# Performance work log

Measured on AMD Instinct MI355X. Metric: run time of the kernel, lower is better.

The kernel has to match this reference:

```python
import jax, jax.numpy as jnp
import numpy as np

B, C, L, D = 8, 16, 512, 256  # batch, channels (attended axis), seq len, d_model


def setup_inputs() -> dict:
    key = jax.random.key(0)
    ks = jax.random.split(key, 9)
    d = D
    x = jax.random.normal(ks[0], (B, C, L, D), dtype=jnp.float32)
    # qkv projection: Linear(d, 3d), xavier_normal weight, zero-ish bias
    Wqkv = jax.random.normal(ks[1], (3 * d, d), dtype=jnp.float32) * (2.0 / (4 * d)) ** 0.5
    bqkv = jnp.zeros((3 * d,), dtype=jnp.float32)
    # additive-attention scorer V: Linear(d, 1)
    Vw = jax.random.normal(ks[2], (1, d), dtype=jnp.float32) * (1.0 / d) ** 0.5
    Vb = jnp.zeros((1,), dtype=jnp.float32)
    bh = jnp.zeros((d,), dtype=jnp.float32)  # nn.Parameter(torch.zeros(d_model))
    ba = jnp.zeros((1,), dtype=jnp.float32)  # nn.Parameter(torch.zeros(1))
    # output projection Linear(d, d)
    Wout = jax.random.normal(ks[3], (d, d), dtype=jnp.float32) * (1.0 / d) ** 0.5
    bout = jnp.zeros((d,), dtype=jnp.float32)
    return {"x": x, "Wqkv": Wqkv, "bqkv": bqkv, "Vw": Vw, "Vb": Vb,
            "bh": bh, "ba": ba, "Wout": Wout, "bout": bout}


def reference(x, Wqkv, bqkv, Vw, Vb, bh, ba, Wout, bout):
    b, c, l, d = x.shape
    # (b, c, l, d) -> (b*l, c, d): attention over the channel axis c per position
    xf = jnp.transpose(x, (0, 2, 1, 3)).reshape(b * l, c, d)
    qkv = xf @ Wqkv.T + bqkv                       # (B, c, 3d)
    q, k, v = jnp.split(qkv, 3, axis=-1)           # each (B, c, d)
    # additive (Bahdanau) score: V(tanh(q_i + k_j + bh)) + ba
    h = jnp.tanh(q[:, :, None, :] + k[:, None, :, :] + bh)  # (B, c, c, d)
    score = jnp.einsum('bqkd,d->bqk', h, Vw[0]) + Vb[0] + ba[0]  # (B, c, c)
    A = jax.nn.softmax(score, axis=-1)             # stable softmax (matches exp(s-max)/sum)
    # torch einsum 'b c c, b c d -> b c d': repeated index -> DIAGONAL of A scales v
    z = jnp.einsum('bcc,bcd->bcd', A, v)           # (B, c, d)
    z = z.reshape(b, l, c, d).transpose(0, 2, 1, 3)  # (b, c, l, d)
    return z @ Wout.T + bout
```

## Files before the change

### kernel.cpp

```cpp
#include <hip/hip_runtime.h>


typedef __attribute__((ext_vector_type(8))) short bf16x8;
typedef __attribute__((ext_vector_type(4))) float f32x4;
typedef __attribute__((ext_vector_type(8))) _Float16 h16x8;
typedef __attribute__((ext_vector_type(4))) _Float16 h16x4;
typedef const __attribute__((address_space(1))) void* gp1_t;
typedef __attribute__((address_space(3))) void* lp3_t;

__device__ __forceinline__ unsigned short f2bf(float f) {
  union { float f; unsigned int u; } v; v.f = f;
  return (unsigned short)((v.u + 0x7FFFu + ((v.u >> 16) & 1u)) >> 16);
}

__device__ __forceinline__ unsigned int cvt_pk_bf16(float a, float b) {
  unsigned int r;
  asm("v_cvt_pk_bf16_f32 %0, %1, %2" : "=v"(r) : "v"(a), "v"(b));
  return r;
}

__global__ __launch_bounds__(256) void ca_prep_kernel(
    const float* __restrict__ Wqkv, const float* __restrict__ Wout,
    const float* __restrict__ bqkv,
    unsigned short* __restrict__ Wqb_t, unsigned short* __restrict__ Wcb_t,
    float* __restrict__ bcomb) {
  const int blk = blockIdx.x;
  if (blk < 64) {
    const int t = blk * 256 + threadIdx.x;
    const int k8 = t >> 9, n = t & 511;
    const float* src = Wqkv + (size_t)n * 256 + k8 * 8;
    const float4 v0 = *(const float4*)src;
    const float4 v1 = *(const float4*)(src + 4);
    bf16x8 o;
    o[0] = (short)f2bf(v0.x); o[1] = (short)f2bf(v0.y);
    o[2] = (short)f2bf(v0.z); o[3] = (short)f2bf(v0.w);
    o[4] = (short)f2bf(v1.x); o[5] = (short)f2bf(v1.y);
    o[6] = (short)f2bf(v1.z); o[7] = (short)f2bf(v1.w);
    *(bf16x8*)(Wqb_t + (size_t)t * 8) = o;
    return;
  }
  const int dp = blk - 64;
  const int e = threadIdx.x;
  const float* wrow = Wout + (size_t)dp * 256;
  float acc = 0.f;
  for (int f = 0; f < 256; ++f)
    acc = fmaf(wrow[f], Wqkv[(size_t)(512 + f) * 256 + e], acc);
  Wcb_t[((size_t)(e >> 3) * 256 + dp) * 8 + (e & 7)] = f2bf(acc);
  if (e == 0) {
    float b = 0.f;
    for (int f = 0; f < 256; ++f) b = fmaf(wrow[f], bqkv[512 + f], b);
    bcomb[dp] = b;
  }
}

__global__ __launch_bounds__(512, 6) void ca_fused(
    const float* __restrict__ x,
    const unsigned short* __restrict__ Wqb_t,
    const unsigned short* __restrict__ Wcb_t,
    const float* __restrict__ bqkv, const float* __restrict__ bh,
    const float* __restrict__ Vw,
    const float* __restrict__ bcomb, const float* __restrict__ bout,
    float* __restrict__ out) {
  __shared__ __align__(16) unsigned short xs[32 * 264];
  __shared__ __align__(16) unsigned short BsEs[16640];
  __shared__ __align__(16) float vw_s[256];
  __shared__ float af_s[32];
  unsigned short* const Bs = BsEs;
  _Float16* const Es = (_Float16*)BsEs;

  const int tid = threadIdx.x;
  const int lane = tid & 63, wave = tid >> 6;
  const int quad = lane >> 4, l15 = lane & 15;
  const int rt0 = blockIdx.x * 32;

  if (tid < 256) vw_s[tid] = -2.f * Vw[tid];

#pragma unroll
  for (int i = 0; i < 4; ++i) {
    const int sb = wave * 256 + i * 64;
    const unsigned short* g = Wqb_t + (size_t)(sb + lane) * 8;
    __builtin_amdgcn_global_load_lds((gp1_t)g, (lp3_t)(Bs + sb * 8), 16, 0, 0);
  }

  {
    const int rl = tid >> 4, c0 = (tid & 15) * 16;
    const int r = rt0 + rl;
    const int b = r >> 13, l = (r >> 4) & 511, c = r & 15;
    const float* src = x + ((size_t)(b * 16 + c) * 512 + l) * 256 + c0;
    unsigned short* dst = xs + rl * 264 + c0;
#pragma unroll
    for (int j = 0; j < 2; ++j) {
      const float4 v0 = *(const float4*)(src + j * 8);
      const float4 v1 = *(const float4*)(src + j * 8 + 4);
      uint4 o;
      o.x = cvt_pk_bf16(v0.x, v0.y);
      o.y = cvt_pk_bf16(v0.z, v0.w);
      o.z = cvt_pk_bf16(v1.x, v1.y);
      o.w = cvt_pk_bf16(v1.z, v1.w);
      *(uint4*)(dst + j * 8) = o;
    }
  }
  __syncthreads();

  f32x4 acc[2][4] = {};
  for (int k0c = 0; k0c < 8; ++k0c) {
    bf16x8 af[2], bfr[4];
#pragma unroll
    for (int mi = 0; mi < 2; ++mi)
      af[mi] = *(const bf16x8*)&xs[(mi * 16 + l15) * 264 + k0c * 32 + quad * 8];
#pragma unroll
    for (int ni = 0; ni < 4; ++ni)
      bfr[ni] = *(const bf16x8*)&Bs[(quad * 512 + wave * 64 + ni * 16 + l15) * 8];
    __syncthreads();
    if (k0c < 7) {
#pragma unroll
      for (int i = 0; i < 4; ++i) {
        const int sb = wave * 256 + i * 64;
        const unsigned short* g =
            Wqb_t + ((size_t)(k0c + 1) * 2048 + sb + lane) * 8;
        __builtin_amdgcn_global_load_lds((gp1_t)g, (lp3_t)(Bs + sb * 8), 16, 0, 0);
      }
    }
#pragma unroll
    for (int mi = 0; mi < 2; ++mi)
#pragma unroll
      for (int ni = 0; ni < 4; ++ni)
        acc[mi][ni] = __builtin_amdgcn_mfma_f32_16x16x32_bf16(
            bfr[ni], af[mi], acc[mi][ni], 0, 0, 0);
    __syncthreads();
  }

  const float SC = 2.8853900817779268f;
  const bool isq = (wave < 4);
#pragma unroll
  for (int mi = 0; mi < 2; ++mi) {
    const int rl = mi * 16 + l15;
#pragma unroll
    for (int ni = 0; ni < 4; ++ni) {
      const int n = wave * 64 + ni * 16 + quad * 4;
      const float4 bq = *(const float4*)(bqkv + n);
      float4 bhv = make_float4(0.f, 0.f, 0.f, 0.f);
      if (isq) bhv = *(const float4*)(bh + n);
      h16x4 st;
      st[0] = (_Float16)__builtin_amdgcn_exp2f(
          fminf(15.f, fmaxf(-15.f, (acc[mi][ni][0] + bq.x + bhv.x) * SC)));
      st[1] = (_Float16)__builtin_amdgcn_exp2f(
          fminf(15.f, fmaxf(-15.f, (acc[mi][ni][1] + bq.y + bhv.y) * SC)));
      st[2] = (_Float16)__builtin_amdgcn_exp2f(
          fminf(15.f, fmaxf(-15.f, (acc[mi][ni][2] + bq.z + bhv.z) * SC)));
      st[3] = (_Float16)__builtin_amdgcn_exp2f(
          fminf(15.f, fmaxf(-15.f, (acc[mi][ni][3] + bq.w + bhv.w) * SC)));
      *(h16x4*)&Es[rl * 520 + n] = st;
    }
  }
  __syncthreads();

  f32x4 acc2[2][2] = {};
  {
    const int p = tid >> 8, qc = (tid >> 4) & 15, kc = tid & 15;
    const _Float16* eqp = Es + (p * 16 + qc) * 520;
    const _Float16* ekp = Es + (p * 16 + kc) * 520 + 256;
    const unsigned short* wb2 = Wcb_t + (size_t)(quad * 256 + wave * 32 + l15) * 8;
    bf16x8 bcur0 = *(const bf16x8*)(wb2);
    bf16x8 bcur1 = *(const bf16x8*)(wb2 + 128);
    f32x4 a4 = {};
#pragma unroll
    for (int c = 0; c < 8; ++c) {
      bf16x8 bnxt0, bnxt1;
      if (c < 7) {
        bnxt0 = *(const bf16x8*)(wb2 + (size_t)(c + 1) * 8192);
        bnxt1 = *(const bf16x8*)(wb2 + (size_t)(c + 1) * 8192 + 128);
      }
      bf16x8 af0 = *(const bf16x8*)&xs[l15 * 264 + c * 32 + quad * 8];
      bf16x8 af1 = *(const bf16x8*)&xs[(16 + l15) * 264 + c * 32 + quad * 8];
#pragma unroll
      for (int j = 0; j < 4; ++j) {
        const int d = c * 32 + j * 8;
        const h16x8 eq = *(const h16x8*)(eqp + d);
        const h16x8 ek = *(const h16x8*)(ekp + d);
        const f32x4 wv0 = *(const f32x4*)(vw_s + d);
        const f32x4 wv1 = *(const f32x4*)(vw_s + d + 4);
        f32x4 sg0, sg1;
        sg0.x = __builtin_amdgcn_rcpf(1.f + (float)eq[0] * (float)ek[0]);
        sg0.y = __builtin_amdgcn_rcpf(1.f + (float)eq[1] * (float)ek[1]);
        sg0.z = __builtin_amdgcn_rcpf(1.f + (float)eq[2] * (float)ek[2]);
        sg0.w = __builtin_amdgcn_rcpf(1.f + (float)eq[3] * (float)ek[3]);
        sg1.x = __builtin_amdgcn_rcpf(1.f + (float)eq[4] * (float)ek[4]);
        sg1.y = __builtin_amdgcn_rcpf(1.f + (float)eq[5] * (float)ek[5]);
        sg1.z = __builtin_amdgcn_rcpf(1.f + (float)eq[6] * (float)ek[6]);
        sg1.w = __builtin_amdgcn_rcpf(1.f + (float)eq[7] * (float)ek[7]);
        a4 += wv0 * sg0 + wv1 * sg1;
      }
      acc2[0][0] = __builtin_amdgcn_mfma_f32_16x16x32_bf16(bcur0, af0, acc2[0][0], 0, 0, 0);
      acc2[0][1] = __builtin_amdgcn_mfma_f32_16x16x32_bf16(bcur1, af0, acc2[0][1], 0, 0, 0);
      acc2[1][0] = __builtin_amdgcn_mfma_f32_16x16x32_bf16(bcur0, af1, acc2[1][0], 0, 0, 0);
      acc2[1][1] = __builtin_amdgcn_mfma_f32_16x16x32_bf16(bcur1, af1, acc2[1][1], 0, 0, 0);
      bcur0 = bnxt0; bcur1 = bnxt1;
    }
    float s = (a4[0] + a4[1]) + (a4[2] + a4[3]);
    float m = s;
    for (int off = 8; off; off >>= 1) m = fmaxf(m, __shfl_xor(m, off, 16));
    const float e = __builtin_amdgcn_exp2f((s - m) * 1.4426950408889634f);
    float sum = e;
    for (int off = 8; off; off >>= 1) sum += __shfl_xor(sum, off, 16);
    if (kc == qc) af_s[p * 16 + qc] = e / sum;
  }
  __syncthreads();

#pragma unroll
  for (int mi = 0; mi < 2; ++mi) {
    const int rl = mi * 16 + l15;
    const int r = rt0 + rl;
    const int c = r & 15, p = r >> 4;
    const int l = p & 511, b = p >> 9;
    const float av = af_s[rl];
    float* orow = out + ((size_t)(b * 16 + c) * 512 + l) * 256;
#pragma unroll
    for (int ni = 0; ni < 2; ++ni) {
      const int n = wave * 32 + ni * 16 + quad * 4;
      const float4 bc = *(const float4*)(bcomb + n);
      const float4 bo = *(const float4*)(bout + n);
      float4 o;
      o.x = fmaf(av, acc2[mi][ni][0] + bc.x, bo.x);
      o.y = fmaf(av, acc2[mi][ni][1] + bc.y, bo.y);
      o.z = fmaf(av, acc2[mi][ni][2] + bc.z, bo.z);
      o.w = fmaf(av, acc2[mi][ni][3] + bc.w, bo.w);
      *(float4*)(orow + n) = o;
    }
  }
}

extern "C" void kernel_launch(void* const* d_in, const int* in_sizes, int n_in,
                              void* d_out, int out_size, void* d_ws, size_t ws_size,
                              hipStream_t stream) {
  (void)in_sizes; (void)n_in; (void)out_size; (void)ws_size;
  const float* x    = (const float*)d_in[0];
  const float* Wqkv = (const float*)d_in[1];
  const float* bqkv = (const float*)d_in[2];
  const float* Vw   = (const float*)d_in[3];
  const float* bh   = (const float*)d_in[5];
  const float* Wout = (const float*)d_in[7];
  const float* bout = (const float*)d_in[8];
  float* out = (float*)d_out;

  float* bcomb = (float*)d_ws;
  unsigned short* Wqb_t = (unsigned short*)(bcomb + 256);
  unsigned short* Wcb_t = Wqb_t + (size_t)512 * 256;

  ca_prep_kernel<<<dim3(320), dim3(256), 0, stream>>>(
      Wqkv, Wout, bqkv, Wqb_t, Wcb_t, bcomb);
  ca_fused<<<dim3(2048), dim3(512), 0, stream>>>(
      x, Wqb_t, Wcb_t, bqkv, bh, Vw, bcomb, bout, out);
}
```

Measured before the change: 190.8 us.

## Batch sigmoid reciprocals via fp16 products and fused combined-bias exponent scaling

```diff
diff --git a/kernel.cpp b/kernel.cpp
--- a/kernel.cpp
+++ b/kernel.cpp
@@ -21,9 +21,9 @@
 
 __global__ __launch_bounds__(256) void ca_prep_kernel(
     const float* __restrict__ Wqkv, const float* __restrict__ Wout,
-    const float* __restrict__ bqkv,
+    const float* __restrict__ bqkv, const float* __restrict__ bh,
     unsigned short* __restrict__ Wqb_t, unsigned short* __restrict__ Wcb_t,
-    float* __restrict__ bcomb) {
+    float* __restrict__ bcomb, float* __restrict__ bsc) {
   const int blk = blockIdx.x;
   if (blk < 64) {
     const int t = blk * 256 + threadIdx.x;
@@ -41,8 +41,14 @@
   }
   const int dp = blk - 64;
   const int e = threadIdx.x;
+  if (dp < 2) {
+    const int n = dp * 256 + e;
+    const float b = bqkv[n] + (n < 256 ? bh[n] : 0.f);
+    bsc[n] = b * 1.4426950408889634f;
+  }
   const float* wrow = Wout + (size_t)dp * 256;
   float acc = 0.f;
+#pragma unroll 8
   for (int f = 0; f < 256; ++f)
     acc = fmaf(wrow[f], Wqkv[(size_t)(512 + f) * 256 + e], acc);
   Wcb_t[((size_t)(e >> 3) * 256 + dp) * 8 + (e & 7)] = f2bf(acc);
@@ -57,7 +63,7 @@
     const float* __restrict__ x,
     const unsigned short* __restrict__ Wqb_t,
     const unsigned short* __restrict__ Wcb_t,
-    const float* __restrict__ bqkv, const float* __restrict__ bh,
+    const float* __restrict__ bsc,
     const float* __restrict__ Vw,
     const float* __restrict__ bcomb, const float* __restrict__ bout,
     float* __restrict__ out) {
@@ -130,26 +136,23 @@
     __syncthreads();
   }
 
-  const float SC = 2.8853900817779268f;
-  const bool isq = (wave < 4);
 #pragma unroll
   for (int mi = 0; mi < 2; ++mi) {
     const int rl = mi * 16 + l15;
 #pragma unroll
     for (int ni = 0; ni < 4; ++ni) {
       const int n = wave * 64 + ni * 16 + quad * 4;
-      const float4 bq = *(const float4*)(bqkv + n);
-      float4 bhv = make_float4(0.f, 0.f, 0.f, 0.f);
-      if (isq) bhv = *(const float4*)(bh + n);
+      const float4 bs = *(const float4*)(bsc + n);
+      const float SC2 = 1.4426950408889634f;
       h16x4 st;
       st[0] = (_Float16)__builtin_amdgcn_exp2f(
-          fminf(15.f, fmaxf(-15.f, (acc[mi][ni][0] + bq.x + bhv.x) * SC)));
+          fminf(7.5f, fmaxf(-7.5f, fmaf(acc[mi][ni][0], SC2, bs.x))));
       st[1] = (_Float16)__builtin_amdgcn_exp2f(
-          fminf(15.f, fmaxf(-15.f, (acc[mi][ni][1] + bq.y + bhv.y) * SC)));
+          fminf(7.5f, fmaxf(-7.5f, fmaf(acc[mi][ni][1], SC2, bs.y))));
       st[2] = (_Float16)__builtin_amdgcn_exp2f(
-          fminf(15.f, fmaxf(-15.f, (acc[mi][ni][2] + bq.z + bhv.z) * SC)));
+          fminf(7.5f, fmaxf(-7.5f, fmaf(acc[mi][ni][2], SC2, bs.z))));
       st[3] = (_Float16)__builtin_amdgcn_exp2f(
-          fminf(15.f, fmaxf(-15.f, (acc[mi][ni][3] + bq.w + bhv.w) * SC)));
+          fminf(7.5f, fmaxf(-7.5f, fmaf(acc[mi][ni][3], SC2, bs.w))));
       *(h16x4*)&Es[rl * 520 + n] = st;
     }
   }
@@ -163,7 +166,7 @@
     const unsigned short* wb2 = Wcb_t + (size_t)(quad * 256 + wave * 32 + l15) * 8;
     bf16x8 bcur0 = *(const bf16x8*)(wb2);
     bf16x8 bcur1 = *(const bf16x8*)(wb2 + 128);
-    f32x4 a4 = {};
+    float asum = 0.f;
 #pragma unroll
     for (int c = 0; c < 8; ++c) {
       bf16x8 bnxt0, bnxt1;
@@ -178,26 +181,41 @@
         const int d = c * 32 + j * 8;
         const h16x8 eq = *(const h16x8*)(eqp + d);
         const h16x8 ek = *(const h16x8*)(ekp + d);
+        const h16x8 pr = eq * ek;
         const f32x4 wv0 = *(const f32x4*)(vw_s + d);
         const f32x4 wv1 = *(const f32x4*)(vw_s + d + 4);
-        f32x4 sg0, sg1;
-        sg0.x = __builtin_amdgcn_rcpf(1.f + (float)eq[0] * (float)ek[0]);
-        sg0.y = __builtin_amdgcn_rcpf(1.f + (float)eq[1] * (float)ek[1]);
-        sg0.z = __builtin_amdgcn_rcpf(1.f + (float)eq[2] * (float)ek[2]);
-        sg0.w = __builtin_amdgcn_rcpf(1.f + (float)eq[3] * (float)ek[3]);
-        sg1.x = __builtin_amdgcn_rcpf(1.f + (float)eq[4] * (float)ek[4]);
-        sg1.y = __builtin_amdgcn_rcpf(1.f + (float)eq[5] * (float)ek[5]);
-        sg1.z = __builtin_amdgcn_rcpf(1.f + (float)eq[6] * (float)ek[6]);
-        sg1.w = __builtin_amdgcn_rcpf(1.f + (float)eq[7] * (float)ek[7]);
-        a4 += wv0 * sg0 + wv1 * sg1;
+        const float p0 = (float)pr[0], p1 = (float)pr[1];
+        const float p2 = (float)pr[2], p3 = (float)pr[3];
+        const float p4 = (float)pr[4], p5 = (float)pr[5];
+        const float p6 = (float)pr[6], p7 = (float)pr[7];
+        const float A0 = fmaf(p0, p0, 1.f), A1 = fmaf(p1, p1, 1.f);
+        const float A2 = fmaf(p2, p2, 1.f), A3 = fmaf(p3, p3, 1.f);
+        const float A4 = fmaf(p4, p4, 1.f), A5 = fmaf(p5, p5, 1.f);
+        const float A6 = fmaf(p6, p6, 1.f), A7 = fmaf(p7, p7, 1.f);
+        {
+          const float P01 = A0 * A1, P23 = A2 * A3;
+          const float i1 = fmaf(wv0.y, A0, wv0.x * A1);
+          const float i2 = fmaf(wv0.w, A2, wv0.z * A3);
+          const float num = fmaf(i2, P01, i1 * P23);
+          asum = fmaf(num, __builtin_amdgcn_rcpf(P01 * P23), asum);
+        }
+        {
+          const float P45 = A4 * A5, P67 = A6 * A7;
+          const float i1 = fmaf(wv1.y, A4, wv1.x * A5);
+          const float i2 = fmaf(wv1.w, A6, wv1.z * A7);
+          const float num = fmaf(i2, P45, i1 * P67);
+          asum = fmaf(num, __builtin_amdgcn_rcpf(P45 * P67), asum);
+        }
       }
+      __builtin_amdgcn_s_setprio(1);
       acc2[0][0] = __builtin_amdgcn_mfma_f32_16x16x32_bf16(bcur0, af0, acc2[0][0], 0, 0, 0);
       acc2[0][1] = __builtin_amdgcn_mfma_f32_16x16x32_bf16(bcur1, af0, acc2[0][1], 0, 0, 0);
       acc2[1][0] = __builtin_amdgcn_mfma_f32_16x16x32_bf16(bcur0, af1, acc2[1][0], 0, 0, 0);
       acc2[1][1] = __builtin_amdgcn_mfma_f32_16x16x32_bf16(bcur1, af1, acc2[1][1], 0, 0, 0);
+      __builtin_amdgcn_s_setprio(0);
       bcur0 = bnxt0; bcur1 = bnxt1;
     }
-    float s = (a4[0] + a4[1]) + (a4[2] + a4[3]);
+    float s = asum;
     float m = s;
     for (int off = 8; off; off >>= 1) m = fmaxf(m, __shfl_xor(m, off, 16));
     const float e = __builtin_amdgcn_exp2f((s - m) * 1.4426950408889634f);
@@ -244,11 +262,12 @@
   float* out = (float*)d_out;
 
   float* bcomb = (float*)d_ws;
-  unsigned short* Wqb_t = (unsigned short*)(bcomb + 256);
+  float* bsc = bcomb + 256;
+  unsigned short* Wqb_t = (unsigned short*)(bsc + 512);
   unsigned short* Wcb_t = Wqb_t + (size_t)512 * 256;
 
   ca_prep_kernel<<<dim3(320), dim3(256), 0, stream>>>(
-      Wqkv, Wout, bqkv, Wqb_t, Wcb_t, bcomb);
+      Wqkv, Wout, bqkv, bh, Wqb_t, Wcb_t, bcomb, bsc);
   ca_fused<<<dim3(2048), dim3(512), 0, stream>>>(
-      x, Wqb_t, Wcb_t, bqkv, bh, Vw, bcomb, bout, out);
-}
+      x, Wqb_t, Wcb_t, bsc, Vw, bcomb, bout, out);
+}
```

After: 309.6 us. 62.3% more time.
